# Kernel optimization log

Measured on AMD Instinct MI355X. Metric: run time of the kernel, lower is better.

The kernel has to match this reference:

```python
import jax, jax.numpy as jnp
import numpy as np

EPS = 1e-12  # F.normalize default eps


def setup_inputs() -> dict:
    key = jax.random.key(0)
    x = jax.random.normal(key, (4, 64, 8192, 1), dtype=jnp.float32)
    return {"x": x, "k": 9, "dilation": 1}


def reference(x, k, dilation):
    # x: (B, D, N, 1)
    B, D, N, _ = x.shape
    kk = k * dilation
    # F.normalize(x, p=2, dim=1)
    norm = jnp.linalg.norm(x, axis=1, keepdims=True)
    xn = x / jnp.maximum(norm, EPS)
    # -> (B, N, D)
    pts = jnp.squeeze(xn, -1).transpose(0, 2, 1)
    # pairwise euclidean distance (cdist p=2)
    sq = jnp.sum(pts * pts, axis=-1)  # (B, N)
    d2 = sq[:, :, None] + sq[:, None, :] - 2.0 * jnp.einsum("bnd,bmd->bnm", pts, pts)
    dist = jnp.sqrt(jnp.maximum(d2, 0.0))  # (B, N, N)
    # torch.topk(-dist, k): k smallest distances
    _, nn_idx = jax.lax.top_k(-dist, kk)  # (B, N, kk)
    center_idx = jnp.broadcast_to(jnp.arange(N, dtype=nn_idx.dtype)[None, :, None], (B, N, kk))
    edge_index = jnp.stack([nn_idx, center_idx], axis=0)  # (2, B, N, kk)
    return edge_index[:, :, :, ::dilation]
```

## Files before the change

kernel.cpp:

```cpp
#include <hip/hip_runtime.h>

#define BB 4
#define DD 64
#define NN 8192
#define KK 9


typedef __attribute__((ext_vector_type(8))) _Float16 f16x8;
typedef __attribute__((ext_vector_type(16))) float f32x16;
typedef __attribute__((ext_vector_type(2))) _Float16 h2;
struct H2x4 { h2 a, b, c, d; };

__device__ __forceinline__ uint4 pack8(const unsigned* w) {
    return make_uint4(w[0] | (w[1] << 16), w[2] | (w[3] << 16),
                      w[4] | (w[5] << 16), w[6] | (w[7] << 16));
}

__device__ __forceinline__ float min3f(float a, float b, float c) {
    return fminf(fminf(a, b), c);
}

__device__ __forceinline__ float dot2acc(h2 g, h2 r, float acc) {
#if __has_builtin(__builtin_amdgcn_fdot2)
    return __builtin_amdgcn_fdot2(g, r, acc, false);
#else
    acc = fmaf((float)g[0], (float)r[0], acc);
    return fmaf((float)g[1], (float)r[1], acc);
#endif
}

__device__ __forceinline__ int s_to_j(int g, int s4) {
    int T = ((g >> 5) << 4) + (g & 15);
    return (T << 5) + ((s4 >> 2) << 3) + (((g >> 4) & 1) << 2) + (s4 & 3);
}

__global__ __launch_bounds__(256) void knorm2_kernel(const float* __restrict__ x,
                                                     float* __restrict__ xnT,
                                                     float* __restrict__ sq,
                                                     unsigned short* __restrict__ Phi,
                                                     unsigned short* __restrict__ Shi) {
    int t = blockIdx.x * 256 + threadIdx.x;
    int b = t >> 13;
    int n = t & (NN - 1);
    const float* xb = x + (size_t)b * DD * NN + n;
    float v[DD];
    float ss = 0.0f;
#pragma unroll
    for (int d = 0; d < DD; ++d) {
        v[d] = xb[(size_t)d * NN];
        ss = fmaf(v[d], v[d], ss);
    }
    float inv = 1.0f / fmaxf(sqrtf(ss), 1e-12f);
    float s2 = 0.0f;
#pragma unroll
    for (int d = 0; d < DD; ++d) {
        v[d] *= inv;
        s2 = fmaf(v[d], v[d], s2);
    }
    sq[t] = s2;
    float4* o4 = reinterpret_cast<float4*>(xnT + (size_t)t * DD);
#pragma unroll
    for (int d = 0; d < DD; d += 4) o4[d >> 2] = make_float4(v[d], v[d+1], v[d+2], v[d+3]);

    size_t base = (size_t)t * DD;
#pragma unroll
    for (int d0 = 0; d0 < DD; d0 += 8) {
        unsigned ph[8], sh[8];
#pragma unroll
        for (int e = 0; e < 8; ++e) {
            float f = v[d0 + e];
            _Float16 hp = (_Float16)f;
            _Float16 hs = (_Float16)(-2.0f * f);
            ph[e] = (unsigned)__builtin_bit_cast(unsigned short, hp);
            sh[e] = (unsigned)__builtin_bit_cast(unsigned short, hs);
        }
        *reinterpret_cast<uint4*>(Phi + base + d0) = pack8(ph);
        *reinterpret_cast<uint4*>(Shi + base + d0) = pack8(sh);
    }
}

__global__ __launch_bounds__(256, 4) void kmin_kernel(const unsigned short* __restrict__ Shi,
                                                      const unsigned short* __restrict__ Phi,
                                                      unsigned short* __restrict__ minbuf16) {
    __shared__ unsigned short Ast[3][2048];
    __shared__ unsigned short stage[4][64][34];
    const int tid = threadIdx.x;
    const int lane = tid & 63;
    const int wave = tid >> 6;
    const int l31 = lane & 31;
    const int half = lane >> 5;
    const int i0 = blockIdx.x * 256 + wave * 64;
    const int b = blockIdx.x >> 5;
    const int jloc0 = blockIdx.y * 512;
    const size_t jrow0 = (size_t)b * NN + jloc0;

    f16x8 Bh0[4], Bh1[4];
    {
        const size_t ib0 = (size_t)(i0 + l31) * DD + half * 8;
        const size_t ib1 = (size_t)(i0 + 32 + l31) * DD + half * 8;
#pragma unroll
        for (int kc = 0; kc < 4; ++kc) {
            Bh0[kc] = *reinterpret_cast<const f16x8*>(Phi + ib0 + kc * 16);
            Bh1[kc] = *reinterpret_cast<const f16x8*>(Phi + ib1 + kc * 16);
        }
    }

    const int srow = tid >> 3;
    const int sp = tid & 7;
    const unsigned soff = (unsigned)(srow * 64 + ((sp * 8) ^ ((srow & 7) << 3)));
    const size_t gbase = (jrow0 + srow) * DD + sp * 8;

    uint4 gA, gB;
    {
        uint4 g0 = *reinterpret_cast<const uint4*>(Shi + gbase);
        *reinterpret_cast<uint4*>(&Ast[0][soff]) = g0;
        gA = *reinterpret_cast<const uint4*>(Shi + gbase + (size_t)1 * 32 * DD);
        gB = *reinterpret_cast<const uint4*>(Shi + gbase + (size_t)2 * 32 * DD);
    }
    __syncthreads();

#pragma unroll 1
    for (int t = 0; t < 16; ++t) {
        const unsigned short* curb = &Ast[t % 3][0];
        f16x8 Ah[4];
#pragma unroll
        for (int kc = 0; kc < 4; ++kc) {
            unsigned off = (unsigned)(l31 * 64 + ((half * 8 + kc * 16) ^ ((l31 & 7) << 3)));
            Ah[kc] = *reinterpret_cast<const f16x8*>(&curb[off]);
        }
        f32x16 c0 = {}, c1 = {};
#pragma unroll
        for (int kc = 0; kc < 4; ++kc)
            c0 = __builtin_amdgcn_mfma_f32_32x32x16_f16(Ah[kc], Bh0[kc], c0, 0, 0, 0);
#pragma unroll
        for (int kc = 0; kc < 4; ++kc)
            c1 = __builtin_amdgcn_mfma_f32_32x32x16_f16(Ah[kc], Bh1[kc], c1, 0, 0, 0);
        const int col = half * 16 + t;
        {
            float q0 = min3f(c0[0], c0[1], c0[2]);
            float q1 = min3f(c0[3], c0[4], c0[5]);
            float q2 = min3f(c0[6], c0[7], c0[8]);
            float q3 = min3f(c0[9], c0[10], c0[11]);
            float q4 = min3f(c0[12], c0[13], c0[14]);
            float mv = fminf(min3f(q0, q1, q2), min3f(q3, q4, c0[15]));
            stage[wave][l31][col] = (unsigned short)__builtin_bit_cast(unsigned short, (_Float16)mv);
        }
        {
            float q0 = min3f(c1[0], c1[1], c1[2]);
            float q1 = min3f(c1[3], c1[4], c1[5]);
            float q2 = min3f(c1[6], c1[7], c1[8]);
            float q3 = min3f(c1[9], c1[10], c1[11]);
            float q4 = min3f(c1[12], c1[13], c1[14]);
            float mv = fminf(min3f(q0, q1, q2), min3f(q3, q4, c1[15]));
            stage[wave][32 + l31][col] = (unsigned short)__builtin_bit_cast(unsigned short, (_Float16)mv);
        }

        if (t < 15)
            *reinterpret_cast<uint4*>(&Ast[(t + 1) % 3][soff]) = gA;
        gA = gB;
        if (t + 3 < 16)
            gB = *reinterpret_cast<const uint4*>(Shi + gbase + (size_t)(t + 3) * 32 * DD);
        __syncthreads();
    }

    unsigned short* dst0 = minbuf16 + (size_t)blockIdx.y * 32;
#pragma unroll
    for (int it = 0; it < 4; ++it) {
        int idx = it * 64 + lane;
        int r = idx >> 2;
        int p = idx & 3;
        const unsigned* s32 = reinterpret_cast<const unsigned*>(&stage[wave][r][p * 8]);
        uint4 vv = make_uint4(s32[0], s32[1], s32[2], s32[3]);
        *reinterpret_cast<uint4*>(dst0 + (size_t)(i0 + r) * 512 + p * 8) = vv;
    }
}

__global__ __launch_bounds__(256) void ksel_kernel(const float* __restrict__ xnT,
                                                   const float* __restrict__ sq,
                                                   const unsigned short* __restrict__ minbuf16,
                                                   const unsigned short* __restrict__ Phi,
                                                   int* __restrict__ out) {
    __shared__ unsigned short glist[4][2][40];
    __shared__ unsigned short jlist[4][2][64];
    const int lane = threadIdx.x & 63;
    const int wave = threadIdx.x >> 6;
    const int tA = __builtin_amdgcn_readfirstlane(blockIdx.x * 8 + wave * 2);
    const int tB = tA + 1;
    const int b = tA >> 13;
    const int nA = tA & (NN - 1);
    const int nB = tB & (NN - 1);

    float gmA[8], gmB[8];
    {
        uint4 a = *reinterpret_cast<const uint4*>(minbuf16 + (size_t)tA * 512 + lane * 8);
        uint4 c = *reinterpret_cast<const uint4*>(minbuf16 + (size_t)tB * 512 + lane * 8);
        unsigned wa[4] = {a.x, a.y, a.z, a.w};
        unsigned wb[4] = {c.x, c.y, c.z, c.w};
#pragma unroll
        for (int q4 = 0; q4 < 4; ++q4) {
            gmA[q4*2+0] = (float)__builtin_bit_cast(_Float16, (unsigned short)(wa[q4] & 0xFFFFu));
            gmA[q4*2+1] = (float)__builtin_bit_cast(_Float16, (unsigned short)(wa[q4] >> 16));
            gmB[q4*2+0] = (float)__builtin_bit_cast(_Float16, (unsigned short)(wb[q4] & 0xFFFFu));
            gmB[q4*2+1] = (float)__builtin_bit_cast(_Float16, (unsigned short)(wb[q4] >> 16));
        }
    }

    float svA = fminf(min3f(gmA[0], gmA[1], gmA[2]),
                      fminf(min3f(gmA[3], gmA[4], gmA[5]), fminf(gmA[6], gmA[7])));
    float svB = fminf(min3f(gmB[0], gmB[1], gmB[2]),
                      fminf(min3f(gmB[3], gmB[4], gmB[5]), fminf(gmB[6], gmB[7])));
#pragma unroll
    for (int k = 2; k <= 64; k <<= 1) {
#pragma unroll
        for (int jj = k >> 1; jj >= 1; jj >>= 1) {
            float oA = __shfl_xor(svA, jj);
            float oB = __shfl_xor(svB, jj);
            bool keepMin = (((lane & jj) == 0) == ((lane & k) == 0));
            svA = keepMin ? fminf(svA, oA) : fmaxf(svA, oA);
            svB = keepMin ? fminf(svB, oB) : fmaxf(svB, oB);
        }
    }
    const float th9pA = __shfl(svA, 8);
    const float th9pB = __shfl(svB, 8);
    const float thetaA  = th9pA + 8e-3f,  thetaB  = th9pB + 8e-3f;
    const float kappa1A = th9pA + 7.5e-3f, kappa1B = th9pB + 7.5e-3f;

    int cntA = 0, cntB = 0;
    unsigned short* glA = &glist[wave][0][0];
    unsigned short* glB = &glist[wave][1][0];
#pragma unroll
    for (int q = 0; q < 8; ++q) {
        bool cA = gmA[q] <= thetaA;
        unsigned long long mA = __ballot(cA);
        int pA = cntA + __popcll(mA & ((1ULL << lane) - 1ULL));
        if (cA && pA < 40) glA[pA] = (unsigned short)(lane * 8 + q);
        cntA += (int)__popcll(mA);
        bool cB = gmB[q] <= thetaB;
        unsigned long long mB = __ballot(cB);
        int pB = cntB + __popcll(mB & ((1ULL << lane) - 1ULL));
        if (cB && pB < 40) glB[pB] = (unsigned short)(lane * 8 + q);
        cntB += (int)__popcll(mB);
    }

    const unsigned short* __restrict__ Pb = Phi + ((size_t)b * NN) * DD;
    H2x4 arhA[8], arhB[8];
    {
        const f16x8* prA = reinterpret_cast<const f16x8*>(Phi + (size_t)tA * DD);
        const f16x8* prB = reinterpret_cast<const f16x8*>(Phi + (size_t)tB * DD);
#pragma unroll
        for (int c8 = 0; c8 < 8; ++c8) {
            arhA[c8] = __builtin_bit_cast(H2x4, prA[c8]);
            arhB[c8] = __builtin_bit_cast(H2x4, prB[c8]);
        }
    }

    const bool ovfA = (cntA > 40), ovfB = (cntB > 40);
    const int totalA = ovfA ? NN : cntA * 16;
    const int totalB = ovfB ? NN : cntB * 16;
    const int nItA = (totalA + 63) >> 6, nItB = (totalB + 63) >> 6;
    const int nIt = nItA > nItB ? nItA : nItB;
    int S1A = 0, S1B = 0;
    unsigned short* jlA = &jlist[wave][0][0];
    unsigned short* jlB = &jlist[wave][1][0];
#pragma unroll 1
    for (int m = 0; m < nIt; ++m) {
        const int idx = m * 64 + lane;
        const bool actA = idx < totalA;
        const bool actB = idx < totalB;
        float m2A = __uint_as_float(0x7f800000u);
        float m2B = __uint_as_float(0x7f800000u);
        int jA = 0, jB = 0;
        if (actA) {
            jA = ovfA ? idx : s_to_j((int)glA[idx >> 4], idx & 15);
            const f16x8* p8 = reinterpret_cast<const f16x8*>(Pb + (size_t)jA * DD);
            float a0 = 0.0f, a1 = 0.0f, a2 = 0.0f, a3 = 0.0f;
#pragma unroll
            for (int c8 = 0; c8 < 8; ++c8) {
                H2x4 g2 = __builtin_bit_cast(H2x4, p8[c8]);
                a0 = dot2acc(g2.a, arhA[c8].a, a0);
                a1 = dot2acc(g2.b, arhA[c8].b, a1);
                a2 = dot2acc(g2.c, arhA[c8].c, a2);
                a3 = dot2acc(g2.d, arhA[c8].d, a3);
            }
            m2A = -2.0f * ((a0 + a1) + (a2 + a3));
        }
        if (actB) {
            jB = ovfB ? idx : s_to_j((int)glB[idx >> 4], idx & 15);
            const f16x8* p8 = reinterpret_cast<const f16x8*>(Pb + (size_t)jB * DD);
            float a0 = 0.0f, a1 = 0.0f, a2 = 0.0f, a3 = 0.0f;
#pragma unroll
            for (int c8 = 0; c8 < 8; ++c8) {
                H2x4 g2 = __builtin_bit_cast(H2x4, p8[c8]);
                a0 = dot2acc(g2.a, arhB[c8].a, a0);
                a1 = dot2acc(g2.b, arhB[c8].b, a1);
                a2 = dot2acc(g2.c, arhB[c8].c, a2);
                a3 = dot2acc(g2.d, arhB[c8].d, a3);
            }
            m2B = -2.0f * ((a0 + a1) + (a2 + a3));
        }
        bool passA = actA && (m2A <= kappa1A);
        unsigned long long mA = __ballot(passA);
        int pA = S1A + __popcll(mA & ((1ULL << lane) - 1ULL));
        if (passA && pA < 64) jlA[pA] = (unsigned short)jA;
        S1A += (int)__popcll(mA);
        bool passB = actB && (m2B <= kappa1B);
        unsigned long long mB = __ballot(passB);
        int pB = S1B + __popcll(mB & ((1ULL << lane) - 1ULL));
        if (passB && pB < 64) jlB[pB] = (unsigned short)jB;
        S1B += (int)__popcll(mB);
    }

    const float* __restrict__ Bb = xnT + (size_t)b * NN * DD;
    const float* __restrict__ sqb = sq + (size_t)b * NN;

    unsigned long long vA = ~0ULL, vB = ~0ULL;
    {
        float4 bufA[4], bufB[4];
        int jA = 0, jB = 0;
        const bool hvA = lane < (S1A <= 64 ? S1A : 64);
        const bool hvB = lane < (S1B <= 64 ? S1B : 64);
        if (hvA) {
            jA = (int)jlA[lane];
            const float4* bc4 = reinterpret_cast<const float4*>(Bb + (size_t)jA * DD);
#pragma unroll
            for (int p = 0; p < 4; ++p) bufA[p] = bc4[p * 4];
        }
        if (hvB) {
            jB = (int)jlB[lane];
            const float4* bc4 = reinterpret_cast<const float4*>(Bb + (size_t)jB * DD);
#pragma unroll
            for (int p = 0; p < 4; ++p) bufB[p] = bc4[p * 4];
        }
        {
            float ar[DD];
            const float4* a4 = reinterpret_cast<const float4*>(xnT + (size_t)tA * DD);
#pragma unroll
            for (int d = 0; d < DD; d += 4) {
                float4 f = a4[d >> 2];
                ar[d] = f.x; ar[d+1] = f.y; ar[d+2] = f.z; ar[d+3] = f.w;
            }
            if (hvA) {
                const float4* bc4 = reinterpret_cast<const float4*>(Bb + (size_t)jA * DD);
                float a0 = 0, a1 = 0, a2 = 0, a3 = 0;
#pragma unroll
                for (int d4 = 0; d4 < 16; ++d4) {
                    float4 f = (d4 % 4 == 0) ? bufA[d4 / 4] : bc4[d4];
                    a0 = fmaf(ar[4*d4+0], f.x, a0);
                    a1 = fmaf(ar[4*d4+1], f.y, a1);
                    a2 = fmaf(ar[4*d4+2], f.z, a2);
                    a3 = fmaf(ar[4*d4+3], f.w, a3);
                }
                float dot = (a0 + a1) + (a2 + a3);
                float key = fmaf(-2.0f, dot, sqb[jA]);
                unsigned ub = __float_as_uint(key);
                ub ^= (0x80000000u | (unsigned)((int)ub >> 31));
                vA = ((unsigned long long)ub << 32) | (unsigned)jA;
            }
        }
        {
            float ar[DD];
            const float4* a4 = reinterpret_cast<const float4*>(xnT + (size_t)tB * DD);
#pragma unroll
            for (int d = 0; d < DD; d += 4) {
                float4 f = a4[d >> 2];
                ar[d] = f.x; ar[d+1] = f.y; ar[d+2] = f.z; ar[d+3] = f.w;
            }
            if (hvB) {
                const float4* bc4 = reinterpret_cast<const float4*>(Bb + (size_t)jB * DD);
                float a0 = 0, a1 = 0, a2 = 0, a3 = 0;
#pragma unroll
                for (int d4 = 0; d4 < 16; ++d4) {
                    float4 f = (d4 % 4 == 0) ? bufB[d4 / 4] : bc4[d4];
                    a0 = fmaf(ar[4*d4+0], f.x, a0);
                    a1 = fmaf(ar[4*d4+1], f.y, a1);
                    a2 = fmaf(ar[4*d4+2], f.z, a2);
                    a3 = fmaf(ar[4*d4+3], f.w, a3);
                }
                float dot = (a0 + a1) + (a2 + a3);
                float key = fmaf(-2.0f, dot, sqb[jB]);
                unsigned ub = __float_as_uint(key);
                ub ^= (0x80000000u | (unsigned)((int)ub >> 31));
                vB = ((unsigned long long)ub << 32) | (unsigned)jB;
            }
        }
    }
#pragma unroll
    for (int k = 2; k <= 64; k <<= 1) {
#pragma unroll
        for (int jj = k >> 1; jj >= 1; jj >>= 1) {
            unsigned long long oA = __shfl_xor(vA, jj);
            unsigned long long oB = __shfl_xor(vB, jj);
            bool keepMin = (((lane & jj) == 0) == ((lane & k) == 0));
            {
                bool less = oA < vA;
                unsigned long long mn = less ? oA : vA;
                unsigned long long mx = less ? vA : oA;
                vA = keepMin ? mn : mx;
            }
            {
                bool less = oB < vB;
                unsigned long long mn = less ? oB : vB;
                unsigned long long mx = less ? vB : oB;
                vB = keepMin ? mn : mx;
            }
        }
    }
    unsigned long long koutA = vA, koutB = vB;

    auto exact_kd = [&](int tX, int totalX, bool ovfX,
                        const unsigned short* glX) -> unsigned long long {
        float ar[DD];
        const float4* a4 = reinterpret_cast<const float4*>(xnT + (size_t)tX * DD);
#pragma unroll
        for (int d = 0; d < DD; d += 4) {
            float4 f = a4[d >> 2];
            ar[d] = f.x; ar[d+1] = f.y; ar[d+2] = f.z; ar[d+3] = f.w;
        }
        unsigned long long kd[KK];
#pragma unroll
        for (int m = 0; m < KK; ++m) kd[m] = ~0ULL;
        const int nI = (totalX + 63) >> 6;
#pragma unroll 1
        for (int m = 0; m < nI; ++m) {
            const int idx = m * 64 + lane;
            if (idx >= totalX) continue;
            int j = ovfX ? idx : s_to_j((int)glX[idx >> 4], idx & 15);
            const float4* bc4 = reinterpret_cast<const float4*>(Bb + (size_t)j * DD);
            float a0 = 0, a1 = 0, a2 = 0, a3 = 0;
#pragma unroll
            for (int d4 = 0; d4 < 16; ++d4) {
                float4 f = bc4[d4];
                a0 = fmaf(ar[4*d4+0], f.x, a0);
                a1 = fmaf(ar[4*d4+1], f.y, a1);
                a2 = fmaf(ar[4*d4+2], f.z, a2);
                a3 = fmaf(ar[4*d4+3], f.w, a3);
            }
            float dot = (a0 + a1) + (a2 + a3);
            float key = fmaf(-2.0f, dot, sqb[j]);
            unsigned ub = __float_as_uint(key);
            ub ^= (0x80000000u | (unsigned)((int)ub >> 31));
            unsigned long long cnd = ((unsigned long long)ub << 32) | (unsigned)j;
            if (cnd < kd[KK - 1]) {
#pragma unroll
                for (int m2 = 0; m2 < KK; ++m2) {
                    bool sw = cnd < kd[m2];
                    unsigned long long lo = sw ? cnd : kd[m2];
                    unsigned long long hi = sw ? kd[m2] : cnd;
                    kd[m2] = lo;
                    cnd = hi;
                }
            }
        }
        unsigned long long ko = ~0ULL;
#pragma unroll
        for (int r = 0; r < KK; ++r) {
            unsigned long long c = kd[0];
            unsigned long long wm = c;
#pragma unroll
            for (int d = 1; d < 64; d <<= 1) {
                unsigned long long o = __shfl_xor(wm, d);
                wm = (o < wm) ? o : wm;
            }
            if (lane == r) ko = wm;
            if (c == wm) {
#pragma unroll
                for (int m2 = 0; m2 < KK - 1; ++m2) kd[m2] = kd[m2 + 1];
                kd[KK - 1] = ~0ULL;
            }
        }
        return ko;
    };
    if (S1A > 64) koutA = exact_kd(tA, totalA, ovfA, glA);
    if (S1B > 64) koutB = exact_kd(tB, totalB, ovfB, glB);

    if (lane < KK) {
        out[(size_t)tA * KK + lane] = (int)(koutA & 0xFFFFFFFFULL);
        out[(size_t)BB * NN * KK + (size_t)tA * KK + lane] = nA;
        out[(size_t)tB * KK + lane] = (int)(koutB & 0xFFFFFFFFULL);
        out[(size_t)BB * NN * KK + (size_t)tB * KK + lane] = nB;
    }
}

__global__ __launch_bounds__(256) void knorm_kernel(const float* __restrict__ x,
                                                    float* __restrict__ xnT,
                                                    float* __restrict__ sq) {
    int t = blockIdx.x * 256 + threadIdx.x;
    int b = t >> 13;
    int n = t & (NN - 1);
    const float* xb = x + (size_t)b * DD * NN + n;
    float v[DD];
    float ss = 0.0f;
#pragma unroll
    for (int d = 0; d < DD; ++d) {
        v[d] = xb[(size_t)d * NN];
        ss = fmaf(v[d], v[d], ss);
    }
    float norm = sqrtf(ss);
    float inv = 1.0f / fmaxf(norm, 1e-12f);
    float s2 = 0.0f;
#pragma unroll
    for (int d = 0; d < DD; ++d) {
        float xv = v[d] * inv;
        v[d] = xv;
        s2 = fmaf(xv, xv, s2);
    }
    float4* o4 = reinterpret_cast<float4*>(xnT + (size_t)t * DD);
#pragma unroll
    for (int d = 0; d < DD; d += 4) {
        o4[d >> 2] = make_float4(v[d], v[d + 1], v[d + 2], v[d + 3]);
    }
    sq[t] = s2;
}

template <int S>
__global__ __launch_bounds__(256, 2) void kdist_kernel(const float* __restrict__ xnT,
                                                       const float* __restrict__ sq,
                                                       unsigned long long* __restrict__ cand) {
    const int rb = blockIdx.x;
    const int b = rb >> 5;
    const int nbase = (rb & 31) * 256;
    const int n = nbase + threadIdx.x;
    const int s = blockIdx.y;
    const int jcount = NN / S;
    const int j0 = s * jcount;
    const int j1 = j0 + jcount;

    const float* __restrict__ Bb = xnT + ((size_t)b * NN) * DD;
    const float* __restrict__ sqb = sq + (size_t)b * NN;

    float ar[DD];
    {
        const float4* a4 = reinterpret_cast<const float4*>(Bb + (size_t)n * DD);
#pragma unroll
        for (int d = 0; d < DD; d += 4) {
            float4 f = a4[d >> 2];
            ar[d] = f.x; ar[d + 1] = f.y; ar[d + 2] = f.z; ar[d + 3] = f.w;
        }
    }
#pragma unroll
    for (int d = 0; d < DD; ++d) {
        asm volatile("" : "+v"(ar[d]));
    }

    unsigned long long kd[KK];
#pragma unroll
    for (int m = 0; m < KK; ++m) kd[m] = ~0ULL;

#pragma unroll 2
    for (int j = j0; j < j1; ++j) {
        const float4* bc4 = reinterpret_cast<const float4*>(Bb + (size_t)j * DD);
        float a0 = 0.0f, a1 = 0.0f, a2 = 0.0f, a3 = 0.0f;
#pragma unroll
        for (int d4 = 0; d4 < DD / 4; ++d4) {
            float4 f = bc4[d4];
            a0 = fmaf(ar[4 * d4 + 0], f.x, a0);
            a1 = fmaf(ar[4 * d4 + 1], f.y, a1);
            a2 = fmaf(ar[4 * d4 + 2], f.z, a2);
            a3 = fmaf(ar[4 * d4 + 3], f.w, a3);
        }
        float dot = (a0 + a1) + (a2 + a3);
        float key = fmaf(-2.0f, dot, sqb[j]);
        unsigned int ub = __float_as_uint(key);
        ub ^= (0x80000000u | (unsigned int)((int)ub >> 31));
        unsigned long long cnd = ((unsigned long long)ub << 32) | (unsigned int)j;
        if (cnd < kd[KK - 1]) {
#pragma unroll
            for (int m = 0; m < KK; ++m) {
                bool sw = cnd < kd[m];
                unsigned long long lo = sw ? cnd : kd[m];
                unsigned long long hi = sw ? kd[m] : cnd;
                kd[m] = lo;
                cnd = hi;
            }
        }
    }

    unsigned long long* outc = cand + ((size_t)(b * NN + n) * S + s) * KK;
#pragma unroll
    for (int m = 0; m < KK; ++m) outc[m] = kd[m];
}

template <int S>
__global__ __launch_bounds__(256) void kmerge_kernel(const unsigned long long* __restrict__ cand,
                                                     int* __restrict__ out) {
    int t = blockIdx.x * 256 + threadIdx.x;
    const unsigned long long* c = cand + (size_t)t * (S * KK);
    unsigned long long kd[KK];
#pragma unroll
    for (int m = 0; m < KK; ++m) kd[m] = ~0ULL;
#pragma unroll
    for (int q = 0; q < S * KK; ++q) {
        unsigned long long cnd = c[q];
        if (cnd < kd[KK - 1]) {
#pragma unroll
            for (int m = 0; m < KK; ++m) {
                bool sw = cnd < kd[m];
                unsigned long long lo = sw ? cnd : kd[m];
                unsigned long long hi = sw ? kd[m] : cnd;
                kd[m] = lo;
                cnd = hi;
            }
        }
    }
    int n = t & (NN - 1);
    int* out0 = out + (size_t)t * KK;
    int* out1 = out + (size_t)BB * NN * KK + (size_t)t * KK;
#pragma unroll
    for (int m = 0; m < KK; ++m) {
        out0[m] = (int)(kd[m] & 0xFFFFFFFFULL);
        out1[m] = n;
    }
}

extern "C" void kernel_launch(void* const* d_in, const int* in_sizes, int n_in,
                              void* d_out, int out_size, void* d_ws, size_t ws_size,
                              hipStream_t stream) {
    const float* x = (const float*)d_in[0];
    int* out = (int*)d_out;
    char* ws = (char*)d_ws;

    constexpr size_t XNT_B = (size_t)BB * NN * DD * 4;
    constexpr size_t SQ_B  = (size_t)BB * NN * 4;
    float* xnT = (float*)ws;
    float* sq  = (float*)(ws + XNT_B);

    constexpr size_t BF_B  = (size_t)BB * NN * DD * 2;
    constexpr size_t OFF_PHI = XNT_B + SQ_B;
    constexpr size_t OFF_PLO = OFF_PHI + BF_B;
    constexpr size_t OFF_SHI = OFF_PLO + BF_B;
    constexpr size_t OFF_SLO = OFF_SHI + BF_B;
    constexpr size_t OFF_MIN = OFF_SLO + BF_B;
    constexpr size_t MIN_B   = (size_t)512 * BB * NN * 4;
    constexpr size_t NEED_NEW = OFF_MIN + MIN_B;

    if (ws_size >= NEED_NEW) {
        unsigned short* Phi = (unsigned short*)(ws + OFF_PHI);
        unsigned short* Shi = (unsigned short*)(ws + OFF_SHI);
        unsigned short* minbuf16 = (unsigned short*)(ws + OFF_MIN);

        knorm2_kernel<<<dim3(BB * NN / 256), dim3(256), 0, stream>>>(x, xnT, sq, Phi, Shi);
        kmin_kernel<<<dim3(BB * NN / 256, 16), dim3(256), 0, stream>>>(Shi, Phi, minbuf16);
        ksel_kernel<<<dim3(BB * NN / 8), dim3(256), 0, stream>>>(xnT, sq, minbuf16, Phi, out);
        return;
    }

    unsigned long long* cand = (unsigned long long*)(ws + XNT_B + SQ_B);
    const size_t base = XNT_B + SQ_B;
    const size_t need8 = base + (size_t)BB * NN * 8 * KK * 8;

    knorm_kernel<<<dim3(BB * NN / 256), dim3(256), 0, stream>>>(x, xnT, sq);
    if (ws_size >= need8) {
        kdist_kernel<8><<<dim3(BB * NN / 256, 8), dim3(256), 0, stream>>>(xnT, sq, cand);
        kmerge_kernel<8><<<dim3(BB * NN / 256), dim3(256), 0, stream>>>(cand, out);
    } else {
        kdist_kernel<4><<<dim3(BB * NN / 256, 4), dim3(256), 0, stream>>>(xnT, sq, cand);
        kmerge_kernel<4><<<dim3(BB * NN / 256), dim3(256), 0, stream>>>(cand, out);
    }
}
```

Before: 213.8 us.

## Outline rare exact top-k fallback and serialize rerank to cut register pressure

```diff
diff --git a/kernel.cpp b/kernel.cpp
--- a/kernel.cpp
+++ b/kernel.cpp
@@ -32,6 +32,74 @@
 __device__ __forceinline__ int s_to_j(int g, int s4) {
     int T = ((g >> 5) << 4) + (g & 15);
     return (T << 5) + ((s4 >> 2) << 3) + (((g >> 4) & 1) << 2) + (s4 & 3);
+}
+
+__device__ __attribute__((noinline))
+unsigned long long exact_kd_fn(const float* __restrict__ xnT,
+                               const float* __restrict__ Bb,
+                               const float* __restrict__ sqb,
+                               int lane, int tX, int totalX, int ovfX,
+                               const unsigned short* glX) {
+    float ar[DD];
+    const float4* a4 = reinterpret_cast<const float4*>(xnT + (size_t)tX * DD);
+#pragma unroll
+    for (int d = 0; d < DD; d += 4) {
+        float4 f = a4[d >> 2];
+        ar[d] = f.x; ar[d+1] = f.y; ar[d+2] = f.z; ar[d+3] = f.w;
+    }
+    unsigned long long kd[KK];
+#pragma unroll
+    for (int m = 0; m < KK; ++m) kd[m] = ~0ULL;
+    const int nI = (totalX + 63) >> 6;
+#pragma unroll 1
+    for (int m = 0; m < nI; ++m) {
+        const int idx = m * 64 + lane;
+        if (idx >= totalX) continue;
+        int j = ovfX ? idx : s_to_j((int)glX[idx >> 4], idx & 15);
+        const float4* bc4 = reinterpret_cast<const float4*>(Bb + (size_t)j * DD);
+        float a0 = 0, a1 = 0, a2 = 0, a3 = 0;
+#pragma unroll
+        for (int d4 = 0; d4 < 16; ++d4) {
+            float4 f = bc4[d4];
+            a0 = fmaf(ar[4*d4+0], f.x, a0);
+            a1 = fmaf(ar[4*d4+1], f.y, a1);
+            a2 = fmaf(ar[4*d4+2], f.z, a2);
+            a3 = fmaf(ar[4*d4+3], f.w, a3);
+        }
+        float dot = (a0 + a1) + (a2 + a3);
+        float key = fmaf(-2.0f, dot, sqb[j]);
+        unsigned ub = __float_as_uint(key);
+        ub ^= (0x80000000u | (unsigned)((int)ub >> 31));
+        unsigned long long cnd = ((unsigned long long)ub << 32) | (unsigned)j;
+        if (cnd < kd[KK - 1]) {
+#pragma unroll
+            for (int m2 = 0; m2 < KK; ++m2) {
+                bool sw = cnd < kd[m2];
+                unsigned long long lo = sw ? cnd : kd[m2];
+                unsigned long long hi = sw ? kd[m2] : cnd;
+                kd[m2] = lo;
+                cnd = hi;
+            }
+        }
+    }
+    unsigned long long ko = ~0ULL;
+#pragma unroll
+    for (int r = 0; r < KK; ++r) {
+        unsigned long long c = kd[0];
+        unsigned long long wm = c;
+#pragma unroll
+        for (int d = 1; d < 64; d <<= 1) {
+            unsigned long long o = __shfl_xor(wm, d);
+            wm = (o < wm) ? o : wm;
+        }
+        if (lane == r) ko = wm;
+        if (c == wm) {
+#pragma unroll
+            for (int m2 = 0; m2 < KK - 1; ++m2) kd[m2] = kd[m2 + 1];
+            kd[KK - 1] = ~0ULL;
+        }
+    }
+    return ko;
 }
 
 __global__ __launch_bounds__(256) void knorm2_kernel(const float* __restrict__ x,
@@ -205,6 +273,18 @@
         }
     }
 
+    const unsigned short* __restrict__ Pb = Phi + ((size_t)b * NN) * DD;
+    H2x4 arhA[8], arhB[8];
+    {
+        const f16x8* prA = reinterpret_cast<const f16x8*>(Phi + (size_t)tA * DD);
+        const f16x8* prB = reinterpret_cast<const f16x8*>(Phi + (size_t)tB * DD);
+#pragma unroll
+        for (int c8 = 0; c8 < 8; ++c8) {
+            arhA[c8] = __builtin_bit_cast(H2x4, prA[c8]);
+            arhB[c8] = __builtin_bit_cast(H2x4, prB[c8]);
+        }
+    }
+
     float svA = fminf(min3f(gmA[0], gmA[1], gmA[2]),
                       fminf(min3f(gmA[3], gmA[4], gmA[5]), fminf(gmA[6], gmA[7])));
     float svB = fminf(min3f(gmB[0], gmB[1], gmB[2]),
@@ -240,18 +320,6 @@
         int pB = cntB + __popcll(mB & ((1ULL << lane) - 1ULL));
         if (cB && pB < 40) glB[pB] = (unsigned short)(lane * 8 + q);
         cntB += (int)__popcll(mB);
-    }
-
-    const unsigned short* __restrict__ Pb = Phi + ((size_t)b * NN) * DD;
-    H2x4 arhA[8], arhB[8];
-    {
-        const f16x8* prA = reinterpret_cast<const f16x8*>(Phi + (size_t)tA * DD);
-        const f16x8* prB = reinterpret_cast<const f16x8*>(Phi + (size_t)tB * DD);
-#pragma unroll
-        for (int c8 = 0; c8 < 8; ++c8) {
-            arhA[c8] = __builtin_bit_cast(H2x4, prA[c8]);
-            arhB[c8] = __builtin_bit_cast(H2x4, prB[c8]);
-        }
     }
 
     const bool ovfA = (cntA > 40), ovfB = (cntB > 40);
@@ -314,76 +382,40 @@
     const float* __restrict__ sqb = sq + (size_t)b * NN;
 
     unsigned long long vA = ~0ULL, vB = ~0ULL;
-    {
-        float4 bufA[4], bufB[4];
-        int jA = 0, jB = 0;
-        const bool hvA = lane < (S1A <= 64 ? S1A : 64);
-        const bool hvB = lane < (S1B <= 64 ? S1B : 64);
-        if (hvA) {
-            jA = (int)jlA[lane];
-            const float4* bc4 = reinterpret_cast<const float4*>(Bb + (size_t)jA * DD);
-#pragma unroll
-            for (int p = 0; p < 4; ++p) bufA[p] = bc4[p * 4];
-        }
-        if (hvB) {
-            jB = (int)jlB[lane];
-            const float4* bc4 = reinterpret_cast<const float4*>(Bb + (size_t)jB * DD);
-#pragma unroll
-            for (int p = 0; p < 4; ++p) bufB[p] = bc4[p * 4];
-        }
-        {
+#pragma unroll 1
+    for (int r = 0; r < 2; ++r) {
+        const int tX = r ? tB : tA;
+        const int S1X = r ? S1B : S1A;
+        const unsigned short* jlX = r ? jlB : jlA;
+        unsigned long long v = ~0ULL;
+        if (lane < (S1X <= 64 ? S1X : 64)) {
+            int j = (int)jlX[lane];
             float ar[DD];
-            const float4* a4 = reinterpret_cast<const float4*>(xnT + (size_t)tA * DD);
+            const float4* a4 = reinterpret_cast<const float4*>(xnT + (size_t)tX * DD);
 #pragma unroll
             for (int d = 0; d < DD; d += 4) {
                 float4 f = a4[d >> 2];
                 ar[d] = f.x; ar[d+1] = f.y; ar[d+2] = f.z; ar[d+3] = f.w;
             }
-            if (hvA) {
-                const float4* bc4 = reinterpret_cast<const float4*>(Bb + (size_t)jA * DD);
-                float a0 = 0, a1 = 0, a2 = 0, a3 = 0;
-#pragma unroll
-                for (int d4 = 0; d4 < 16; ++d4) {
-                    float4 f = (d4 % 4 == 0) ? bufA[d4 / 4] : bc4[d4];
-                    a0 = fmaf(ar[4*d4+0], f.x, a0);
-                    a1 = fmaf(ar[4*d4+1], f.y, a1);
-                    a2 = fmaf(ar[4*d4+2], f.z, a2);
-                    a3 = fmaf(ar[4*d4+3], f.w, a3);
-                }
-                float dot = (a0 + a1) + (a2 + a3);
-                float key = fmaf(-2.0f, dot, sqb[jA]);
-                unsigned ub = __float_as_uint(key);
-                ub ^= (0x80000000u | (unsigned)((int)ub >> 31));
-                vA = ((unsigned long long)ub << 32) | (unsigned)jA;
-            }
-        }
-        {
-            float ar[DD];
-            const float4* a4 = reinterpret_cast<const float4*>(xnT + (size_t)tB * DD);
-#pragma unroll
-            for (int d = 0; d < DD; d += 4) {
-                float4 f = a4[d >> 2];
-                ar[d] = f.x; ar[d+1] = f.y; ar[d+2] = f.z; ar[d+3] = f.w;
-            }
-            if (hvB) {
-                const float4* bc4 = reinterpret_cast<const float4*>(Bb + (size_t)jB * DD);
-                float a0 = 0, a1 = 0, a2 = 0, a3 = 0;
-#pragma unroll
-                for (int d4 = 0; d4 < 16; ++d4) {
-                    float4 f = (d4 % 4 == 0) ? bufB[d4 / 4] : bc4[d4];
-                    a0 = fmaf(ar[4*d4+0], f.x, a0);
-                    a1 = fmaf(ar[4*d4+1], f.y, a1);
-                    a2 = fmaf(ar[4*d4+2], f.z, a2);
-                    a3 = fmaf(ar[4*d4+3], f.w, a3);
-                }
-                float dot = (a0 + a1) + (a2 + a3);
-                float key = fmaf(-2.0f, dot, sqb[jB]);
-                unsigned ub = __float_as_uint(key);
-                ub ^= (0x80000000u | (unsigned)((int)ub >> 31));
-                vB = ((unsigned long long)ub << 32) | (unsigned)jB;
-            }
-        }
-    }
+            const float4* bc4 = reinterpret_cast<const float4*>(Bb + (size_t)j * DD);
+            float a0 = 0, a1 = 0, a2 = 0, a3 = 0;
+#pragma unroll
+            for (int d4 = 0; d4 < 16; ++d4) {
+                float4 f = bc4[d4];
+                a0 = fmaf(ar[4*d4+0], f.x, a0);
+                a1 = fmaf(ar[4*d4+1], f.y, a1);
+                a2 = fmaf(ar[4*d4+2], f.z, a2);
+                a3 = fmaf(ar[4*d4+3], f.w, a3);
+            }
+            float dot = (a0 + a1) + (a2 + a3);
+            float key = fmaf(-2.0f, dot, sqb[j]);
+            unsigned ub = __float_as_uint(key);
+            ub ^= (0x80000000u | (unsigned)((int)ub >> 31));
+            v = ((unsigned long long)ub << 32) | (unsigned)j;
+        }
+        if (r == 0) vA = v; else vB = v;
+    }
+
 #pragma unroll
     for (int k = 2; k <= 64; k <<= 1) {
 #pragma unroll
@@ -407,71 +439,8 @@
     }
     unsigned long long koutA = vA, koutB = vB;
 
-    auto exact_kd = [&](int tX, int totalX, bool ovfX,
-                        const unsigned short* glX) -> unsigned long long {
-        float ar[DD];
-        const float4* a4 = reinterpret_cast<const float4*>(xnT + (size_t)tX * DD);
-#pragma unroll
-        for (int d = 0; d < DD; d += 4) {
-            float4 f = a4[d >> 2];
-            ar[d] = f.x; ar[d+1] = f.y; ar[d+2] = f.z; ar[d+3] = f.w;
-        }
-        unsigned long long kd[KK];
-#pragma unroll
-        for (int m = 0; m < KK; ++m) kd[m] = ~0ULL;
-        const int nI = (totalX + 63) >> 6;
-#pragma unroll 1
-        for (int m = 0; m < nI; ++m) {
-            const int idx = m * 64 + lane;
-            if (idx >= totalX) continue;
-            int j = ovfX ? idx : s_to_j((int)glX[idx >> 4], idx & 15);
-            const float4* bc4 = reinterpret_cast<const float4*>(Bb + (size_t)j * DD);
-            float a0 = 0, a1 = 0, a2 = 0, a3 = 0;
-#pragma unroll
-            for (int d4 = 0; d4 < 16; ++d4) {
-                float4 f = bc4[d4];
-                a0 = fmaf(ar[4*d4+0], f.x, a0);
-                a1 = fmaf(ar[4*d4+1], f.y, a1);
-                a2 = fmaf(ar[4*d4+2], f.z, a2);
-                a3 = fmaf(ar[4*d4+3], f.w, a3);
-            }
-            float dot = (a0 + a1) + (a2 + a3);
-            float key = fmaf(-2.0f, dot, sqb[j]);
-            unsigned ub = __float_as_uint(key);
-            ub ^= (0x80000000u | (unsigned)((int)ub >> 31));
-            unsigned long long cnd = ((unsigned long long)ub << 32) | (unsigned)j;
-            if (cnd < kd[KK - 1]) {
-#pragma unroll
-                for (int m2 = 0; m2 < KK; ++m2) {
-                    bool sw = cnd < kd[m2];
-                    unsigned long long lo = sw ? cnd : kd[m2];
-                    unsigned long long hi = sw ? kd[m2] : cnd;
-                    kd[m2] = lo;
-                    cnd = hi;
-                }
-            }
-        }
-        unsigned long long ko = ~0ULL;
-#pragma unroll
-        for (int r = 0; r < KK; ++r) {
-            unsigned long long c = kd[0];
-            unsigned long long wm = c;
-#pragma unroll
-            for (int d = 1; d < 64; d <<= 1) {
-                unsigned long long o = __shfl_xor(wm, d);
-                wm = (o < wm) ? o : wm;
-            }
-            if (lane == r) ko = wm;
-            if (c == wm) {
-#pragma unroll
-                for (int m2 = 0; m2 < KK - 1; ++m2) kd[m2] = kd[m2 + 1];
-                kd[KK - 1] = ~0ULL;
-            }
-        }
-        return ko;
-    };
-    if (S1A > 64) koutA = exact_kd(tA, totalA, ovfA, glA);
-    if (S1B > 64) koutB = exact_kd(tB, totalB, ovfB, glB);
+    if (S1A > 64) koutA = exact_kd_fn(xnT, Bb, sqb, lane, tA, totalA, (int)ovfA, glA);
+    if (S1B > 64) koutB = exact_kd_fn(xnT, Bb, sqb, lane, tB, totalB, (int)ovfB, glB);
 
     if (lane < KK) {
         out[(size_t)tA * KK + lane] = (int)(koutA & 0xFFFFFFFFULL);
```

Result: slower. 238.1 us (+11.4%).
